# Optimization experiments

Hardware: AMD Instinct MI355X
Metric: run time of the kernel (lower is better)

## Reference

```python
import jax, jax.numpy as jnp
import numpy as np

MAP_CHANNEL_WEIGHT = 50.0
PATCH = 3  # unfold kernel size and stride (stride == kernel -> non-overlapping)


def setup_inputs() -> dict:
    key = jax.random.key(0)
    k1, k2, k3, k4 = jax.random.split(key, 4)
    style_resp = jax.random.normal(k1, (1, 256, 256, 256), dtype=jnp.float32)
    style_map = jax.random.uniform(k2, (1, 3, 1024, 1024), dtype=jnp.float32)
    output_map = jax.random.uniform(k3, (1, 3, 1024, 1024), dtype=jnp.float32)
    model_resp = jax.random.normal(k4, (1, 256, 256, 256), dtype=jnp.float32)
    return {"style_resp": style_resp, "style_map": style_map,
            "output_map": output_map, "model_resp": model_resp}


def _avg_pool(x, d):
    # x: (N, C, H, W) -> AvgPool2d((d, d)) with default stride = kernel
    n, c, h, w = x.shape
    return x.reshape(n, c, h // d, d, w // d, d).mean(axis=(3, 5))


def _unfold(x):
    # x: (C, H, W) -> (C*3*3, P) matching torch.nn.Unfold((3,3), stride=3)
    # block layout along dim 0 is (C, kh, kw); patches are row-major.
    c, h, w = x.shape
    nh = (h - PATCH) // PATCH + 1
    nw = (w - PATCH) // PATCH + 1
    x = x[:, : nh * PATCH, : nw * PATCH].reshape(c, nh, PATCH, nw, PATCH)
    x = x.transpose(0, 2, 4, 1, 3)  # (C, kh, kw, nh, nw)
    return x.reshape(c * PATCH * PATCH, nh * nw)


def reference(style_resp, style_map, output_map, model_resp):
    # --- init-time precomputation (faithful to __init__) ---
    channel_count = style_resp.shape[0]  # original code uses dim 0 (batch) here
    patch_height = style_resp.shape[2]
    down = style_map.shape[2] // patch_height
    style_map_down = _avg_pool(style_map, down)
    output_map_down = _avg_pool(output_map, down)
    sr = jnp.concatenate(
        [style_resp, MAP_CHANNEL_WEIGHT * style_map_down * channel_count], axis=1)
    style_patches = _unfold(sr[0])                      # (D, P)
    style_norm_inv = 1.0 / jnp.linalg.norm(style_patches, axis=0)  # (P,)

    # --- loss(model_response) ---
    img = jnp.concatenate(
        [model_resp, MAP_CHANNEL_WEIGHT * output_map_down * channel_count], axis=1)
    img_patches = _unfold(img[0])                       # (D, P)
    img_norm_inv = 1.0 / jnp.linalg.norm(img_patches, axis=0)      # (P,)

    # Faithful to original: sim = ((img^T @ style) * img_norm[j]).T * style_norm[j]
    # => C[i, j] = <img_j, style_i> * img_norm_inv[i] * style_norm_inv[j]
    sim = jnp.einsum('di,dj->ij', style_patches, img_patches)  # (P, P): <style_i, img_j>
    sim = sim * img_norm_inv[:, None] * style_norm_inv[None, :]
    nearest = jnp.argmax(sim, axis=1)                   # (P,)

    matched = style_patches[:, nearest]                 # (D, P)
    loss = jnp.mean((img_patches - matched) ** 2)
    return loss
```

## Files before the change

kernel.cpp:

```cpp
#include <hip/hip_runtime.h>
#include <float.h>
#include <math.h>

#define D_REAL 2331
#define D_PAD  2336
#define DQ     2304
#define N_REAL 7225
#define N_PAD  7424
#define NT     29

typedef __attribute__((ext_vector_type(8))) short bf16x8_t;
typedef __attribute__((ext_vector_type(4))) float f32x4_t;
typedef __attribute__((ext_vector_type(8))) int   v8i_t;
typedef __attribute__((ext_vector_type(4))) int   v4i_t;

__device__ __forceinline__ unsigned short f2bf(float x) {
    union { float f; unsigned int u; } v; v.f = x;
    unsigned int r = v.u + 0x7FFFu + ((v.u >> 16) & 1u);
    return (unsigned short)(r >> 16);
}
__device__ __forceinline__ float bflo(unsigned int u) {
    union { unsigned int x; float f; } v; v.x = u << 16; return v.f;
}
__device__ __forceinline__ float bfhi(unsigned int u) {
    union { unsigned int x; float f; } v; v.x = u & 0xFFFF0000u; return v.f;
}

#define GLOAD_LDS16(g, l) __builtin_amdgcn_global_load_lds( \
    (const __attribute__((address_space(1))) void*)(g),     \
    (__attribute__((address_space(3))) void*)(l), 16, 0, 0)

__global__ __launch_bounds__(256) void build_all(
        const float* __restrict__ respS, const float* __restrict__ respI,
        const float* __restrict__ mapS,  const float* __restrict__ mapI,
        unsigned short* __restrict__ PbS, unsigned short* __restrict__ PbI,
        unsigned char* __restrict__ PqS, unsigned char* __restrict__ PqI) {
    const int mat = blockIdx.y;
    unsigned short* Pb = mat ? PbI : PbS;
    const int bx = blockIdx.x;
    if (bx < 6120) {
        const float* resp = mat ? respI : respS;
        unsigned char* Pq = mat ? PqI : PqS;
        __shared__ float slab[5 * 768];
        const int u  = bx / 72;
        const int d0 = (bx - u * 72) * 32;
        const int c0 = d0 / 9;
        const int cN = (d0 + 31) / 9 - c0 + 1;
        const int total = cN * 768;
        for (int idx = threadIdx.x; idx < total; idx += 256) {
            int cc = idx / 768;
            int rem = idx - cc * 768;
            slab[idx] = resp[(((size_t)(c0 + cc)) << 16) + ((size_t)(3 * u) << 8) + rem];
        }
        __syncthreads();
        const int dl16 = threadIdx.x & 15;
        const int de = d0 + 2 * dl16, dq = de + 1;
        const int ce = de / 9, re = de - ce * 9, pe = re / 3, qe = re - pe * 3;
        const int co = dq / 9, ro = dq - co * 9, po = ro / 3, qo = ro - po * 3;
        const int base_e = (ce - c0) * 768 + pe * 256 + qe;
        const int base_o = (co - c0) * 768 + po * 256 + qo;
        const int v0 = threadIdx.x >> 4;
        for (int v = v0; v < 85; v += 16) {
            float x0 = slab[base_e + 3 * v];
            float x1 = slab[base_o + 3 * v];
            size_t row = (size_t)(u * 85 + v);
            *(unsigned int*)&Pb[row * D_PAD + de] =
                (unsigned int)f2bf(x0) | ((unsigned int)f2bf(x1) << 16);
            int pk = __builtin_amdgcn_cvt_pk_fp8_f32(x0, x1, 0, false);
            *(unsigned short*)&Pq[row * DQ + de] = (unsigned short)pk;
        }
    } else {
        const float* map = mat ? mapI : mapS;
        int t = (bx - 6120) * 256 + threadIdx.x;
        int n = t >> 5, dm = t & 31;
        if (n >= N_REAL) return;
        float val = 0.f;
        if (dm < 27) {
            int u = n / 85, v = n - u * 85;
            int ch = dm / 9, r9 = dm - ch * 9, p = r9 / 3, q = r9 - p * 3;
            const float* mp = map + ((size_t)ch << 20)
                                  + ((size_t)((3 * u + p) * 4) << 10)
                                  + (size_t)((3 * v + q) * 4);
            float s = 0.f;
            #pragma unroll
            for (int a = 0; a < 4; a++)
                #pragma unroll
                for (int b = 0; b < 4; b++) s += mp[a * 1024 + b];
            val = 3.125f * s;
        }
        Pb[(size_t)n * D_PAD + 2304 + dm] = f2bf(val);
    }
}

__global__ __launch_bounds__(256) void col_norms(const unsigned short* __restrict__ Sb,
                                                 float* __restrict__ sinv,
                                                 double* __restrict__ accum) {
    if (blockIdx.x == 0 && threadIdx.x == 0) *accum = 0.0;
    int n = blockIdx.x * 4 + (threadIdx.x >> 6);
    int lane = threadIdx.x & 63;
    const uint4* sp = (const uint4*)(Sb + (size_t)n * D_PAD);
    float s = 0.f;
    for (int k = lane; k < D_PAD / 8; k += 64) {
        uint4 a = sp[k];
        float x0 = bflo(a.x), x1 = bfhi(a.x), x2 = bflo(a.y), x3 = bfhi(a.y);
        float x4 = bflo(a.z), x5 = bfhi(a.z), x6 = bflo(a.w), x7 = bfhi(a.w);
        s = fmaf(x0, x0, s); s = fmaf(x1, x1, s);
        s = fmaf(x2, x2, s); s = fmaf(x3, x3, s);
        s = fmaf(x4, x4, s); s = fmaf(x5, x5, s);
        s = fmaf(x6, x6, s); s = fmaf(x7, x7, s);
    }
    #pragma unroll
    for (int off = 32; off > 0; off >>= 1) s += __shfl_xor(s, off);
    if (lane == 0) sinv[n] = (n < N_REAL) ? rsqrtf(s) : 0.f;
}

__global__ __launch_bounds__(512, 2) void gemm_argmax(
        const unsigned char* __restrict__ Sq, const unsigned char* __restrict__ Iq,
        const unsigned short* __restrict__ Sb, const unsigned short* __restrict__ Ib,
        const float* __restrict__ sinv,
        float* __restrict__ pval, int* __restrict__ pidx) {
    const int bid = blockIdx.x;
    const int it = bid % NT, jt = bid / NT;
    const int i0 = it * 256, j0 = jt * 256;

    __shared__ __align__(16) unsigned char Af[2][256][128];
    __shared__ __align__(16) unsigned char Bf[2][256][128];

    const int tid = threadIdx.x;
    const int L = tid & 63, w = tid >> 6;
    const int wr = w >> 2, wc = w & 3;
    const int m = L & 15, q = L >> 4;
    const int clo = ((2 * q)     ^ (m & 7)) << 4;
    const int chi = ((2 * q + 1) ^ (m & 7)) << 4;

    f32x4_t acc[8][4];
    #pragma unroll
    for (int a = 0; a < 8; a++)
        #pragma unroll
        for (int b = 0; b < 4; b++) acc[a][b] = (f32x4_t){0.f, 0.f, 0.f, 0.f};

    const int aro = 128 * (w >> 2) + 8 * (w & 3);
    const int bro = 8 * w;
    const unsigned char* pA = Sq + (size_t)(i0 + aro + (L >> 3)) * DQ
                            + (((L & 7) ^ (L >> 3)) << 4);
    const unsigned char* pB = Iq + (size_t)(j0 + bro + (L >> 3)) * DQ
                            + (((L & 7) ^ (L >> 3)) << 4);

#define STG_A(s, ko, b) GLOAD_LDS16(pA + (size_t)(32 * (s)) * DQ + (ko), \
                                    &Af[b][32 * (s) + aro][0])
#define STG_B(s, ko, b) GLOAD_LDS16(pB + (size_t)(64 * (s)) * DQ + (ko), \
                                    &Bf[b][64 * (s) + bro][0])

#define LDA8(dst, b, mi) {                                              \
    const unsigned char* p_ = &Af[b][wr * 128 + (mi) * 16 + m][0];      \
    v4i_t lo_ = *(const v4i_t*)(p_ + clo);                              \
    v4i_t hi_ = *(const v4i_t*)(p_ + chi);                              \
    dst = __builtin_shufflevector(lo_, hi_, 0, 1, 2, 3, 4, 5, 6, 7); }
#define LDB8(dst, b, nj) {                                              \
    const unsigned char* p_ = &Bf[b][wc * 64 + (nj) * 16 + m][0];       \
    v4i_t lo_ = *(const v4i_t*)(p_ + clo);                              \
    v4i_t hi_ = *(const v4i_t*)(p_ + chi);                              \
    dst = __builtin_shufflevector(lo_, hi_, 0, 1, 2, 3, 4, 5, 6, 7); }

#define RDB4(b) LDB8(bq0, b, 0) LDB8(bq1, b, 1) LDB8(bq2, b, 2) LDB8(bq3, b, 3)

#define MXMFMA(a, b, c) __builtin_amdgcn_mfma_scale_f32_16x16x128_f8f6f4( \
    a, b, c, 0, 0, 0, 0x7F, 0, 0x7F)

#define PHASE(b, p2, RDB, STAGES, TAILW) {                              \
    v8i_t a0_, a1_;                                                     \
    RDB                                                                 \
    LDA8(a0_, b, 2 * (p2))                                              \
    LDA8(a1_, b, 2 * (p2) + 1)                                          \
    STAGES                                                              \
    __builtin_amdgcn_sched_barrier(0);                                  \
    __builtin_amdgcn_s_barrier();                                       \
    asm volatile("s_waitcnt lgkmcnt(0)" ::: "memory");                  \
    __builtin_amdgcn_sched_barrier(0);                                  \
    __builtin_amdgcn_s_setprio(1);                                      \
    acc[2*(p2)  ][0] = MXMFMA(a0_, bq0, acc[2*(p2)  ][0]);              \
    acc[2*(p2)  ][1] = MXMFMA(a0_, bq1, acc[2*(p2)  ][1]);              \
    acc[2*(p2)  ][2] = MXMFMA(a0_, bq2, acc[2*(p2)  ][2]);              \
    acc[2*(p2)  ][3] = MXMFMA(a0_, bq3, acc[2*(p2)  ][3]);              \
    acc[2*(p2)+1][0] = MXMFMA(a1_, bq0, acc[2*(p2)+1][0]);              \
    acc[2*(p2)+1][1] = MXMFMA(a1_, bq1, acc[2*(p2)+1][1]);              \
    acc[2*(p2)+1][2] = MXMFMA(a1_, bq2, acc[2*(p2)+1][2]);              \
    acc[2*(p2)+1][3] = MXMFMA(a1_, bq3, acc[2*(p2)+1][3]);              \
    __builtin_amdgcn_s_setprio(0);                                      \
    __builtin_amdgcn_sched_barrier(0);                                  \
    TAILW                                                               \
    __builtin_amdgcn_s_barrier();                                       \
}

    v8i_t bq0, bq1, bq2, bq3;

    STG_B(0, 0, 0); STG_A(0, 0, 0);
    STG_B(1, 0, 0); STG_A(1, 0, 0);
    STG_B(2, 0, 0); STG_A(2, 0, 0);
    STG_B(3, 0, 0); STG_A(3, 0, 0);
    STG_B(0, 128, 1); STG_A(0, 128, 1);
    STG_B(1, 128, 1); STG_A(1, 128, 1);
    STG_B(2, 128, 1); STG_A(2, 128, 1);
    asm volatile("s_waitcnt vmcnt(6)" ::: "memory");
    __builtin_amdgcn_s_barrier();

    #pragma unroll 1
    for (int i8 = 0; i8 < 8; ++i8) {
        PHASE(0, 0, RDB4(0), STG_B(3, 128, 1); STG_A(3, 128, 1);, )
        PHASE(0, 1, ,        STG_B(0, 256, 0); STG_A(0, 256, 0);, )
        PHASE(0, 2, ,        STG_B(1, 256, 0); STG_A(1, 256, 0);, )
        PHASE(0, 3, ,        STG_B(2, 256, 0); STG_A(2, 256, 0);,
              asm volatile("s_waitcnt vmcnt(6)" ::: "memory");)
        PHASE(1, 0, RDB4(1), STG_B(3, 256, 0); STG_A(3, 256, 0);, )
        PHASE(1, 1, ,        STG_B(0, 384, 1); STG_A(0, 384, 1);, )
        PHASE(1, 2, ,        STG_B(1, 384, 1); STG_A(1, 384, 1);, )
        PHASE(1, 3, ,        STG_B(2, 384, 1); STG_A(2, 384, 1);,
              asm volatile("s_waitcnt vmcnt(6)" ::: "memory");)
        pA += 256; pB += 256;
    }

    unsigned short (*At)[32] = (unsigned short(*)[32])&Af[0][0][0];
    unsigned short (*Bt)[32] = (unsigned short(*)[32])&Bf[0][0][0];
    const unsigned short* ptA = Sb + (size_t)(i0 + 16 * w + (L >> 2)) * D_PAD
                              + 2304 + (((L & 3) ^ ((L >> 3) & 3)) << 3);
    const unsigned short* ptB = Ib + (size_t)(j0 + 16 * w + (L >> 2)) * D_PAD
                              + 2304 + (((L & 3) ^ ((L >> 3) & 3)) << 3);

    PHASE(0, 0, RDB4(0), STG_B(3, 128, 1); STG_A(3, 128, 1);, )
    PHASE(0, 1, , , )
    PHASE(0, 2, , , )
    PHASE(0, 3, , , asm volatile("s_waitcnt vmcnt(0)" ::: "memory");)
    PHASE(1, 0, RDB4(1), GLOAD_LDS16(ptA, &At[16 * w][0]);, )
    PHASE(1, 1, , GLOAD_LDS16(ptA + (size_t)128 * D_PAD, &At[128 + 16 * w][0]);, )
    PHASE(1, 2, , GLOAD_LDS16(ptB, &Bt[16 * w][0]);, )
    PHASE(1, 3, , GLOAD_LDS16(ptB + (size_t)128 * D_PAD, &Bt[128 + 16 * w][0]);,
          asm volatile("s_waitcnt vmcnt(0)" ::: "memory");)
#undef PHASE
#undef RDB4
#undef STG_A
#undef STG_B

    {
        const int cht = (q ^ ((m >> 1) & 3)) << 3;
        bf16x8_t bt[4];
        #pragma unroll
        for (int nj = 0; nj < 4; nj++)
            bt[nj] = *(const bf16x8_t*)&Bt[wc * 64 + nj * 16 + m][cht];
        #pragma unroll
        for (int mi = 0; mi < 8; mi++) {
            bf16x8_t a_ = *(const bf16x8_t*)&At[wr * 128 + mi * 16 + m][cht];
            #pragma unroll
            for (int nj = 0; nj < 4; nj++)
                acc[mi][nj] = __builtin_amdgcn_mfma_f32_16x16x32_bf16(
                    a_, bt[nj], acc[mi][nj], 0, 0, 0);
        }
    }

    float sjv[4];
    #pragma unroll
    for (int nj = 0; nj < 4; nj++) sjv[nj] = sinv[j0 + wc * 64 + nj * 16 + m];
    #pragma unroll
    for (int mi = 0; mi < 8; mi++) {
        #pragma unroll
        for (int r = 0; r < 4; r++) {
            float best = -INFINITY; int bidx = 0x7fffffff;
            #pragma unroll
            for (int nj = 0; nj < 4; nj++) {
                int j = j0 + wc * 64 + nj * 16 + m;
                float v = (j < N_REAL) ? acc[mi][nj][r] * sjv[nj] : -INFINITY;
                if (v > best) { best = v; bidx = j; }
            }
            #pragma unroll
            for (int off = 1; off < 16; off <<= 1) {
                float ov = __shfl_xor(best, off);
                int   oi = __shfl_xor(bidx, off);
                if (ov > best || (ov == best && oi < bidx)) { best = ov; bidx = oi; }
            }
            if (m == 0) {
                int i = i0 + wr * 128 + mi * 16 + q * 4 + r;
                pval[(size_t)jt * N_PAD + i] = best;
                pidx[(size_t)jt * N_PAD + i] = bidx;
            }
        }
    }
}

__global__ __launch_bounds__(256) void loss_kernel(
        const unsigned short* __restrict__ Ib, const unsigned short* __restrict__ Sb,
        const float* __restrict__ pval, const int* __restrict__ pidx,
        double* __restrict__ accum) {
    __shared__ float wsum[4];
    __shared__ int sjn;
    const int n = blockIdx.x;
    if (threadIdx.x < 64) {
        float v = -INFINITY; int id = 0x7fffffff;
        if (threadIdx.x < NT) {
            v  = pval[(size_t)threadIdx.x * N_PAD + n];
            id = pidx[(size_t)threadIdx.x * N_PAD + n];
        }
        #pragma unroll
        for (int off = 32; off > 0; off >>= 1) {
            float ov = __shfl_xor(v, off);
            int   oi = __shfl_xor(id, off);
            if (ov > v || (ov == v && oi < id)) { v = ov; id = oi; }
        }
        if (threadIdx.x == 0) sjn = id;
    }
    __syncthreads();
    const int jn = sjn;
    const uint4* ip = (const uint4*)(Ib + (size_t)n  * D_PAD);
    const uint4* sp = (const uint4*)(Sb + (size_t)jn * D_PAD);
    float s = 0.f;
    for (int k = threadIdx.x; k < D_PAD / 8; k += 256) {
        uint4 a = ip[k], b = sp[k];
        float d0 = bflo(a.x) - bflo(b.x), d1 = bfhi(a.x) - bfhi(b.x);
        float d2 = bflo(a.y) - bflo(b.y), d3 = bfhi(a.y) - bfhi(b.y);
        float d4 = bflo(a.z) - bflo(b.z), d5 = bfhi(a.z) - bfhi(b.z);
        float d6 = bflo(a.w) - bflo(b.w), d7 = bfhi(a.w) - bfhi(b.w);
        s = fmaf(d0, d0, s); s = fmaf(d1, d1, s);
        s = fmaf(d2, d2, s); s = fmaf(d3, d3, s);
        s = fmaf(d4, d4, s); s = fmaf(d5, d5, s);
        s = fmaf(d6, d6, s); s = fmaf(d7, d7, s);
    }
    #pragma unroll
    for (int off = 32; off > 0; off >>= 1) s += __shfl_xor(s, off);
    int lane = threadIdx.x & 63, wv = threadIdx.x >> 6;
    if (lane == 0) wsum[wv] = s;
    __syncthreads();
    if (threadIdx.x == 0) {
        double t = (double)wsum[0] + (double)wsum[1] + (double)wsum[2] + (double)wsum[3];
        atomicAdd(accum, t);
    }
}

__global__ void finalize(const double* __restrict__ accum, float* __restrict__ out) {
    out[0] = (float)(accum[0] / (double)((long long)D_REAL * N_REAL));
}

extern "C" void kernel_launch(void* const* d_in, const int* in_sizes, int n_in,
                              void* d_out, int out_size, void* d_ws, size_t ws_size,
                              hipStream_t stream) {
    const float* style_resp = (const float*)d_in[0];
    const float* style_map  = (const float*)d_in[1];
    const float* output_map = (const float*)d_in[2];
    const float* model_resp = (const float*)d_in[3];
    float* out = (float*)d_out;

    unsigned short* Sb = (unsigned short*)d_ws;
    unsigned short* Ib = Sb + (size_t)D_PAD * N_PAD;
    unsigned char*  Sq = (unsigned char*)(Ib + (size_t)D_PAD * N_PAD);
    unsigned char*  Iq = Sq + (size_t)DQ * N_PAD;
    float* sinv    = (float*)(Iq + (size_t)DQ * N_PAD);
    float* pval    = sinv + N_PAD;
    int*   pidx    = (int*)(pval + (size_t)NT * N_PAD);
    double* accum  = (double*)(pidx + (size_t)NT * N_PAD);

    build_all<<<dim3(6120 + 904, 2), 256, 0, stream>>>(
        style_resp, model_resp, style_map, output_map, Sb, Ib, Sq, Iq);

    col_norms<<<N_PAD / 4, 256, 0, stream>>>(Sb, sinv, accum);

    gemm_argmax<<<NT * NT, 512, 0, stream>>>(Sq, Iq, Sb, Ib, sinv, pval, pidx);

    loss_kernel<<<N_REAL, 256, 0, stream>>>(Ib, Sb, pval, pidx, accum);
    finalize<<<1, 1, 0, stream>>>(accum, out);
}
```

Measured before the change: 501.4 us.

## Shrink GEMM-argmax tiles to 128x128 with four blocks per CU

```diff
diff --git a/kernel.cpp b/kernel.cpp
--- a/kernel.cpp
+++ b/kernel.cpp
@@ -6,8 +6,9 @@
 #define D_PAD  2336
 #define DQ     2304
 #define N_REAL 7225
-#define N_PAD  7424
-#define NT     29
+#define N_PAD  7296
+#define JTILES 57
+#define ITILES 57
 
 typedef __attribute__((ext_vector_type(8))) short bf16x8_t;
 typedef __attribute__((ext_vector_type(4))) float f32x4_t;
@@ -114,17 +115,17 @@
     if (lane == 0) sinv[n] = (n < N_REAL) ? rsqrtf(s) : 0.f;
 }
 
-__global__ __launch_bounds__(512, 2) void gemm_argmax(
+__global__ __launch_bounds__(512, 4) void gemm_argmax(
         const unsigned char* __restrict__ Sq, const unsigned char* __restrict__ Iq,
         const unsigned short* __restrict__ Sb, const unsigned short* __restrict__ Ib,
         const float* __restrict__ sinv,
         float* __restrict__ pval, int* __restrict__ pidx) {
     const int bid = blockIdx.x;
-    const int it = bid % NT, jt = bid / NT;
-    const int i0 = it * 256, j0 = jt * 256;
-
-    __shared__ __align__(16) unsigned char Af[2][256][128];
-    __shared__ __align__(16) unsigned char Bf[2][256][128];
+    const int it = bid % ITILES, jt = bid / ITILES;
+    const int i0 = it * 128, j0 = jt * 128;
+
+    __shared__ __align__(16) unsigned char Af[2][128][128];
+    __shared__ __align__(16) unsigned char Bf[2][128][128];
 
     const int tid = threadIdx.x;
     const int L = tid & 63, w = tid >> 6;
@@ -133,89 +134,76 @@
     const int clo = ((2 * q)     ^ (m & 7)) << 4;
     const int chi = ((2 * q + 1) ^ (m & 7)) << 4;
 
-    f32x4_t acc[8][4];
+    f32x4_t acc[4][2];
     #pragma unroll
-    for (int a = 0; a < 8; a++)
+    for (int a = 0; a < 4; a++)
         #pragma unroll
-        for (int b = 0; b < 4; b++) acc[a][b] = (f32x4_t){0.f, 0.f, 0.f, 0.f};
-
-    const int aro = 128 * (w >> 2) + 8 * (w & 3);
-    const int bro = 8 * w;
-    const unsigned char* pA = Sq + (size_t)(i0 + aro + (L >> 3)) * DQ
-                            + (((L & 7) ^ (L >> 3)) << 4);
-    const unsigned char* pB = Iq + (size_t)(j0 + bro + (L >> 3)) * DQ
-                            + (((L & 7) ^ (L >> 3)) << 4);
-
-#define STG_A(s, ko, b) GLOAD_LDS16(pA + (size_t)(32 * (s)) * DQ + (ko), \
-                                    &Af[b][32 * (s) + aro][0])
-#define STG_B(s, ko, b) GLOAD_LDS16(pB + (size_t)(64 * (s)) * DQ + (ko), \
-                                    &Bf[b][64 * (s) + bro][0])
-
-#define LDA8(dst, b, mi) {                                              \
-    const unsigned char* p_ = &Af[b][wr * 128 + (mi) * 16 + m][0];      \
-    v4i_t lo_ = *(const v4i_t*)(p_ + clo);                              \
-    v4i_t hi_ = *(const v4i_t*)(p_ + chi);                              \
+        for (int b = 0; b < 2; b++) acc[a][b] = (f32x4_t){0.f, 0.f, 0.f, 0.f};
+
+    const int r8 = 8 * w + (L >> 3);
+    const int swz = ((L & 7) ^ (L >> 3)) << 4;
+    const unsigned char* pA = Sq + (size_t)(i0 + r8 + (r8 & 32)) * DQ + swz;
+    const unsigned char* pB = Iq + (size_t)(j0 + r8) * DQ + swz;
+
+#define STG_A(h, ko, b) GLOAD_LDS16(pA + (size_t)(32 * (h)) * DQ + (ko), \
+                                    &Af[b][64 * (h) + 8 * w][0])
+#define STG_B(h, ko, b) GLOAD_LDS16(pB + (size_t)(64 * (h)) * DQ + (ko), \
+                                    &Bf[b][64 * (h) + 8 * w][0])
+
+#define LDA8(dst, b, mi) {                                                    \
+    const unsigned char* p_ =                                                 \
+        &Af[b][(((mi) >> 1) << 6) + (wr << 5) + (((mi) & 1) << 4) + m][0];    \
+    v4i_t lo_ = *(const v4i_t*)(p_ + clo);                                    \
+    v4i_t hi_ = *(const v4i_t*)(p_ + chi);                                    \
     dst = __builtin_shufflevector(lo_, hi_, 0, 1, 2, 3, 4, 5, 6, 7); }
-#define LDB8(dst, b, nj) {                                              \
-    const unsigned char* p_ = &Bf[b][wc * 64 + (nj) * 16 + m][0];       \
-    v4i_t lo_ = *(const v4i_t*)(p_ + clo);                              \
-    v4i_t hi_ = *(const v4i_t*)(p_ + chi);                              \
+#define LDB8(dst, b, nj) {                                                    \
+    const unsigned char* p_ = &Bf[b][(wc << 5) + ((nj) << 4) + m][0];         \
+    v4i_t lo_ = *(const v4i_t*)(p_ + clo);                                    \
+    v4i_t hi_ = *(const v4i_t*)(p_ + chi);                                    \
     dst = __builtin_shufflevector(lo_, hi_, 0, 1, 2, 3, 4, 5, 6, 7); }
 
-#define RDB4(b) LDB8(bq0, b, 0) LDB8(bq1, b, 1) LDB8(bq2, b, 2) LDB8(bq3, b, 3)
+#define RDB2(b) LDB8(bq0, b, 0) LDB8(bq1, b, 1)
 
 #define MXMFMA(a, b, c) __builtin_amdgcn_mfma_scale_f32_16x16x128_f8f6f4( \
     a, b, c, 0, 0, 0, 0x7F, 0, 0x7F)
 
-#define PHASE(b, p2, RDB, STAGES, TAILW) {                              \
+#define GATE3 asm volatile("s_waitcnt vmcnt(3)" ::: "memory");
+#define GATE0 asm volatile("s_waitcnt vmcnt(0)" ::: "memory");
+
+#define PHASE(b, h, RDB, STAGES, GATE) {                                \
     v8i_t a0_, a1_;                                                     \
     RDB                                                                 \
-    LDA8(a0_, b, 2 * (p2))                                              \
-    LDA8(a1_, b, 2 * (p2) + 1)                                          \
+    LDA8(a0_, b, 2 * (h))                                               \
+    LDA8(a1_, b, 2 * (h) + 1)                                           \
     STAGES                                                              \
     __builtin_amdgcn_sched_barrier(0);                                  \
     __builtin_amdgcn_s_barrier();                                       \
     asm volatile("s_waitcnt lgkmcnt(0)" ::: "memory");                  \
     __builtin_amdgcn_sched_barrier(0);                                  \
     __builtin_amdgcn_s_setprio(1);                                      \
-    acc[2*(p2)  ][0] = MXMFMA(a0_, bq0, acc[2*(p2)  ][0]);              \
-    acc[2*(p2)  ][1] = MXMFMA(a0_, bq1, acc[2*(p2)  ][1]);              \
-    acc[2*(p2)  ][2] = MXMFMA(a0_, bq2, acc[2*(p2)  ][2]);              \
-    acc[2*(p2)  ][3] = MXMFMA(a0_, bq3, acc[2*(p2)  ][3]);              \
-    acc[2*(p2)+1][0] = MXMFMA(a1_, bq0, acc[2*(p2)+1][0]);              \
-    acc[2*(p2)+1][1] = MXMFMA(a1_, bq1, acc[2*(p2)+1][1]);              \
-    acc[2*(p2)+1][2] = MXMFMA(a1_, bq2, acc[2*(p2)+1][2]);              \
-    acc[2*(p2)+1][3] = MXMFMA(a1_, bq3, acc[2*(p2)+1][3]);              \
+    acc[2*(h)  ][0] = MXMFMA(a0_, bq0, acc[2*(h)  ][0]);                \
+    acc[2*(h)  ][1] = MXMFMA(a0_, bq1, acc[2*(h)  ][1]);                \
+    acc[2*(h)+1][0] = MXMFMA(a1_, bq0, acc[2*(h)+1][0]);                \
+    acc[2*(h)+1][1] = MXMFMA(a1_, bq1, acc[2*(h)+1][1]);                \
     __builtin_amdgcn_s_setprio(0);                                      \
     __builtin_amdgcn_sched_barrier(0);                                  \
-    TAILW                                                               \
+    GATE                                                                \
     __builtin_amdgcn_s_barrier();                                       \
 }
 
-    v8i_t bq0, bq1, bq2, bq3;
-
-    STG_B(0, 0, 0); STG_A(0, 0, 0);
-    STG_B(1, 0, 0); STG_A(1, 0, 0);
-    STG_B(2, 0, 0); STG_A(2, 0, 0);
-    STG_B(3, 0, 0); STG_A(3, 0, 0);
-    STG_B(0, 128, 1); STG_A(0, 128, 1);
-    STG_B(1, 128, 1); STG_A(1, 128, 1);
-    STG_B(2, 128, 1); STG_A(2, 128, 1);
-    asm volatile("s_waitcnt vmcnt(6)" ::: "memory");
+    v8i_t bq0, bq1;
+
+    STG_B(0, 0, 0); STG_B(1, 0, 0); STG_A(0, 0, 0); STG_A(1, 0, 0);
+    STG_B(0, 128, 1); STG_B(1, 128, 1); STG_A(0, 128, 1);
+    GATE3
     __builtin_amdgcn_s_barrier();
 
     #pragma unroll 1
-    for (int i8 = 0; i8 < 8; ++i8) {
-        PHASE(0, 0, RDB4(0), STG_B(3, 128, 1); STG_A(3, 128, 1);, )
-        PHASE(0, 1, ,        STG_B(0, 256, 0); STG_A(0, 256, 0);, )
-        PHASE(0, 2, ,        STG_B(1, 256, 0); STG_A(1, 256, 0);, )
-        PHASE(0, 3, ,        STG_B(2, 256, 0); STG_A(2, 256, 0);,
-              asm volatile("s_waitcnt vmcnt(6)" ::: "memory");)
-        PHASE(1, 0, RDB4(1), STG_B(3, 256, 0); STG_A(3, 256, 0);, )
-        PHASE(1, 1, ,        STG_B(0, 384, 1); STG_A(0, 384, 1);, )
-        PHASE(1, 2, ,        STG_B(1, 384, 1); STG_A(1, 384, 1);, )
-        PHASE(1, 3, ,        STG_B(2, 384, 1); STG_A(2, 384, 1);,
-              asm volatile("s_waitcnt vmcnt(6)" ::: "memory");)
+    for (int p = 0; p < 8; ++p) {
+        PHASE(0, 0, RDB2(0), STG_A(1, 128, 1);, )
+        PHASE(0, 1, ,        STG_B(0, 256, 0); STG_B(1, 256, 0); STG_A(0, 256, 0);, GATE3)
+        PHASE(1, 0, RDB2(1), STG_A(1, 256, 0);, )
+        PHASE(1, 1, ,        STG_B(0, 384, 1); STG_B(1, 384, 1); STG_A(0, 384, 1);, GATE3)
         pA += 256; pB += 256;
     }
 
@@ -226,48 +214,44 @@
     const unsigned short* ptB = Ib + (size_t)(j0 + 16 * w + (L >> 2)) * D_PAD
                               + 2304 + (((L & 3) ^ ((L >> 3) & 3)) << 3);
 
-    PHASE(0, 0, RDB4(0), STG_B(3, 128, 1); STG_A(3, 128, 1);, )
-    PHASE(0, 1, , , )
-    PHASE(0, 2, , , )
-    PHASE(0, 3, , , asm volatile("s_waitcnt vmcnt(0)" ::: "memory");)
-    PHASE(1, 0, RDB4(1), GLOAD_LDS16(ptA, &At[16 * w][0]);, )
-    PHASE(1, 1, , GLOAD_LDS16(ptA + (size_t)128 * D_PAD, &At[128 + 16 * w][0]);, )
-    PHASE(1, 2, , GLOAD_LDS16(ptB, &Bt[16 * w][0]);, )
-    PHASE(1, 3, , GLOAD_LDS16(ptB + (size_t)128 * D_PAD, &Bt[128 + 16 * w][0]);,
-          asm volatile("s_waitcnt vmcnt(0)" ::: "memory");)
+    PHASE(0, 0, RDB2(0), STG_A(1, 128, 1);, )
+    PHASE(0, 1, , , GATE0)
+    PHASE(1, 0, RDB2(1),
+          GLOAD_LDS16(ptA, &At[16 * w][0]);
+          GLOAD_LDS16(ptB, &Bt[16 * w][0]);, )
+    PHASE(1, 1, , , GATE0)
 #undef PHASE
-#undef RDB4
+#undef RDB2
 #undef STG_A
 #undef STG_B
 
     {
         const int cht = (q ^ ((m >> 1) & 3)) << 3;
-        bf16x8_t bt[4];
+        bf16x8_t bt0 = *(const bf16x8_t*)&Bt[(wc << 5) + m][cht];
+        bf16x8_t bt1 = *(const bf16x8_t*)&Bt[(wc << 5) + 16 + m][cht];
         #pragma unroll
-        for (int nj = 0; nj < 4; nj++)
-            bt[nj] = *(const bf16x8_t*)&Bt[wc * 64 + nj * 16 + m][cht];
-        #pragma unroll
-        for (int mi = 0; mi < 8; mi++) {
-            bf16x8_t a_ = *(const bf16x8_t*)&At[wr * 128 + mi * 16 + m][cht];
-            #pragma unroll
-            for (int nj = 0; nj < 4; nj++)
-                acc[mi][nj] = __builtin_amdgcn_mfma_f32_16x16x32_bf16(
-                    a_, bt[nj], acc[mi][nj], 0, 0, 0);
-        }
-    }
-
-    float sjv[4];
+        for (int mi = 0; mi < 4; mi++) {
+            bf16x8_t a_ = *(const bf16x8_t*)&At[(wr << 6) + mi * 16 + m][cht];
+            acc[mi][0] = __builtin_amdgcn_mfma_f32_16x16x32_bf16(
+                a_, bt0, acc[mi][0], 0, 0, 0);
+            acc[mi][1] = __builtin_amdgcn_mfma_f32_16x16x32_bf16(
+                a_, bt1, acc[mi][1], 0, 0, 0);
+        }
+    }
+
+    const float sj0 = sinv[j0 + (wc << 5) + m];
+    const float sj1 = sinv[j0 + (wc << 5) + 16 + m];
     #pragma unroll
-    for (int nj = 0; nj < 4; nj++) sjv[nj] = sinv[j0 + wc * 64 + nj * 16 + m];
-    #pragma unroll
-    for (int mi = 0; mi < 8; mi++) {
+    for (int mi = 0; mi < 4; mi++) {
         #pragma unroll
         for (int r = 0; r < 4; r++) {
             float best = -INFINITY; int bidx = 0x7fffffff;
-            #pragma unroll
-            for (int nj = 0; nj < 4; nj++) {
-                int j = j0 + wc * 64 + nj * 16 + m;
-                float v = (j < N_REAL) ? acc[mi][nj][r] * sjv[nj] : -INFINITY;
+            {
+                int j = j0 + (wc << 5) + m;
+                float v = (j < N_REAL) ? acc[mi][0][r] * sj0 : -INFINITY;
+                if (v > best) { best = v; bidx = j; }
+                j += 16;
+                v = (j < N_REAL) ? acc[mi][1][r] * sj1 : -INFINITY;
                 if (v > best) { best = v; bidx = j; }
             }
             #pragma unroll
@@ -277,7 +261,7 @@
                 if (ov > best || (ov == best && oi < bidx)) { best = ov; bidx = oi; }
             }
             if (m == 0) {
-                int i = i0 + wr * 128 + mi * 16 + q * 4 + r;
+                int i = i0 + (wr << 6) + mi * 16 + (q << 2) + r;
                 pval[(size_t)jt * N_PAD + i] = best;
                 pidx[(size_t)jt * N_PAD + i] = bidx;
             }
@@ -294,7 +278,7 @@
     const int n = blockIdx.x;
     if (threadIdx.x < 64) {
         float v = -INFINITY; int id = 0x7fffffff;
-        if (threadIdx.x < NT) {
+        if (threadIdx.x < JTILES) {
             v  = pval[(size_t)threadIdx.x * N_PAD + n];
             id = pidx[(size_t)threadIdx.x * N_PAD + n];
         }
@@ -352,15 +336,15 @@
     unsigned char*  Iq = Sq + (size_t)DQ * N_PAD;
     float* sinv    = (float*)(Iq + (size_t)DQ * N_PAD);
     float* pval    = sinv + N_PAD;
-    int*   pidx    = (int*)(pval + (size_t)NT * N_PAD);
-    double* accum  = (double*)(pidx + (size_t)NT * N_PAD);
+    int*   pidx    = (int*)(pval + (size_t)JTILES * N_PAD);
+    double* accum  = (double*)(pidx + (size_t)JTILES * N_PAD);
 
     build_all<<<dim3(6120 + 904, 2), 256, 0, stream>>>(
         style_resp, model_resp, style_map, output_map, Sb, Ib, Sq, Iq);
 
     col_norms<<<N_PAD / 4, 256, 0, stream>>>(Sb, sinv, accum);
 
-    gemm_argmax<<<NT * NT, 512, 0, stream>>>(Sq, Iq, Sb, Ib, sinv, pval, pidx);
+    gemm_argmax<<<ITILES * JTILES, 512, 0, stream>>>(Sq, Iq, Sb, Ib, sinv, pval, pidx);
 
     loss_kernel<<<N_REAL, 256, 0, stream>>>(Ib, Sb, pval, pidx, accum);
     finalize<<<1, 1, 0, stream>>>(accum, out);
```

After: 498.1 us. About the same (-0.7%).
